# Performance work log

Measured on AMD Instinct MI355X. Metric: run time of the kernel, lower is better.

## Reference

```python
import jax, jax.numpy as jnp
import numpy as np

B, T, K = 256, 1024, 128


def setup_inputs() -> dict:
    key = jax.random.key(0)
    k1, k2, k3, k4, k5 = jax.random.split(key, 5)
    EMISSIONS = jax.random.normal(k1, (B, T, K), dtype=jnp.float32)
    TAGS = jax.random.randint(k2, (B, T), 0, K, dtype=jnp.int64)
    MASK = jnp.ones((B, T), dtype=bool)
    START = jax.random.normal(k3, (K,), dtype=jnp.float32) * 0.01
    END = jax.random.normal(k4, (K,), dtype=jnp.float32) * 0.01
    TRANS = jax.random.normal(k5, (K, K), dtype=jnp.float32) * 0.01
    return {"EMISSIONS": EMISSIONS, "TAGS": TAGS, "MASK": MASK,
            "START": START, "END": END, "TRANS": TRANS}


def _forward_logz(emissions, mask, start, end, trans):
    # emissions (B,T,K), mask (B,T) bool -> logZ (B,)
    alpha0 = start[None, :] + emissions[:, 0, :]  # (B,K)

    def step(alpha, inp):
        emit, m = inp  # emit (B,K), m (B,) bool
        # PACK[b,i,j] = alpha[b,i] + trans[i,j]; logsumexp over prev tag i
        new = jax.nn.logsumexp(alpha[:, :, None] + trans[None, :, :], axis=1) + emit
        alpha = jnp.where(m[:, None], new, alpha)
        return alpha, None

    xs = (jnp.swapaxes(emissions[:, 1:, :], 0, 1),  # (T-1,B,K)
          jnp.swapaxes(mask[:, 1:], 0, 1))          # (T-1,B)
    alphaT, _ = jax.lax.scan(step, alpha0, xs)
    return jax.nn.logsumexp(alphaT + end[None, :], axis=1)


def _gold_score(emissions, tags, mask, start, end, trans):
    b = emissions.shape[0]
    ba = jnp.arange(b)
    maskf = mask.astype(emissions.dtype)
    sc0 = (start[tags[:, 0]] + emissions[ba, 0, tags[:, 0]]) * maskf[:, 0]
    pr = jnp.maximum(tags[:, :-1], 0)  # clamp(min=0)
    cr = jnp.maximum(tags[:, 1:], 0)
    m = (mask[:, 1:] & mask[:, :-1]).astype(emissions.dtype)  # (B,T-1)
    trans_sc = trans[pr, cr]  # (B,T-1)
    emit_sc = jnp.take_along_axis(emissions[:, 1:, :], cr[:, :, None], axis=2)[:, :, 0]
    sc = sc0 + jnp.sum((trans_sc + emit_sc) * m, axis=1)
    lenm1 = jnp.sum(mask.astype(jnp.int32), axis=1) - 1
    last = tags[ba, lenm1]
    return sc + end[last]


def reference(EMISSIONS, TAGS, MASK, START, END, TRANS):
    logz = _forward_logz(EMISSIONS, MASK, START, END, TRANS)
    gold = _gold_score(EMISSIONS, TAGS, MASK, START, END, TRANS)
    return jnp.mean(logz - gold)
```

## Files before the change

kernel.cpp:

```cpp
#include <hip/hip_runtime.h>
#include <math.h>

#define Bn 256
#define Tn 1024
#define Kn 128
#define NT 256
#define CH 16
#define CHF (CH * Kn)
#define USTR 36
#define UW (4 * USTR)
#define UIDX(j) (((j) >> 5) * USTR + ((j) & 31))

__global__ __launch_bounds__(NT, 1) void crf_fwd_kernel(
    const float* __restrict__ emis,
    const int*   __restrict__ tags,
    const float* __restrict__ startv,
    const float* __restrict__ endv,
    const float* __restrict__ trans,
    float* __restrict__ per_b)
{
    const int b    = blockIdx.x;
    const int tid  = threadIdx.x;
    const int wave = tid >> 6;
    const int lane = tid & 63;
    const int g4   = lane >> 2;
    const int q    = lane & 3;
    const int c0   = wave * 32 + g4 * 2;
    const bool wrt = (q == 0);
    const int wslot = wave * USTR + 2 * g4;
    const int ubase = q * USTR;

    __shared__ __align__(16) float U[2 * UW];
    __shared__ __align__(16) float Xs[2 * CHF];
    __shared__ float red[NT];

    const float* eb = emis + (size_t)b * Tn * Kn;
    const int*   tb = tags + b * Tn;

    const float* tp = trans + (size_t)(32 * q) * Kn + c0;
    float4 F0, F1, F2, F3, F4, F5, F6, F7, F8, F9, F10, F11, F12, F13, F14, F15;
#define LDE(k, Fk)                                                  \
    {                                                               \
        float2 ea = *(const float2*)(tp + (size_t)(2 * k) * Kn);    \
        float2 ec = *(const float2*)(tp + (size_t)(2 * k + 1) * Kn);\
        Fk = make_float4(__expf(ea.x), __expf(ea.y),                \
                         __expf(ec.x), __expf(ec.y));               \
    }
    LDE(0, F0)   LDE(1, F1)   LDE(2, F2)   LDE(3, F3)
    LDE(4, F4)   LDE(5, F5)   LDE(6, F6)   LDE(7, F7)
    LDE(8, F8)   LDE(9, F9)   LDE(10, F10) LDE(11, F11)
    LDE(12, F12) LDE(13, F13) LDE(14, F14) LDE(15, F15)
#undef LDE

    float gl = 0.f;
    for (int t = 1 + tid; t < Tn; t += NT) {
        int pt = tb[t - 1];
        int ct = tb[t];
        gl += trans[pt * Kn + ct] + eb[(size_t)t * Kn + ct];
    }
    if (tid == 0) {
        int t0 = tb[0];
        gl += startv[t0] + eb[t0] + endv[tb[Tn - 1]];
    }
    red[tid] = gl;

    {
        const float4* e4 = (const float4*)(eb + Kn);
        float4 a = e4[tid];
        float4 d = e4[tid + NT];
        ((float4*)Xs)[tid] =
            make_float4(__expf(a.x), __expf(a.y), __expf(a.z), __expf(a.w));
        ((float4*)Xs)[tid + NT] =
            make_float4(__expf(d.x), __expf(d.y), __expf(d.z), __expf(d.w));
    }
    if (tid < Kn) {
        U[UW + UIDX(tid)] = __expf(startv[tid] + eb[tid]);
    }
    __syncthreads();

#pragma unroll
    for (int s = NT / 2; s > 0; s >>= 1) {
        if (tid < s) red[tid] += red[tid + s];
        __syncthreads();
    }
    const float gold = red[0];

    float  base = 0.f;
    float4 pf0  = make_float4(0, 0, 0, 0);
    float4 pf1  = make_float4(0, 0, 0, 0);

#define DOT2A(qa, qb, Fk)                      \
    aa0 = fmaf(qa, Fk.x, aa0);                 \
    aa1 = fmaf(qa, Fk.y, aa1);                 \
    ab0 = fmaf(qb, Fk.z, ab0);                 \
    ab1 = fmaf(qb, Fk.w, ab1);
#define DOT2B(qa, qb, Fk)                      \
    ba0 = fmaf(qa, Fk.x, ba0);                 \
    ba1 = fmaf(qa, Fk.y, ba1);                 \
    bb0 = fmaf(qb, Fk.z, bb0);                 \
    bb1 = fmaf(qb, Fk.w, bb1);

#define STEP(RB, SLOT, NORM)                                               \
    {                                                                      \
        const float4* Up4 = (const float4*)&U[(RB) * UW + ubase];          \
        float4 v0 = Up4[0], v1 = Up4[1], v2 = Up4[2], v3 = Up4[3];         \
        float4 v4 = Up4[4], v5 = Up4[5], v6 = Up4[6], v7 = Up4[7];         \
        float2 xr = *(const float2*)&Xc[(SLOT) * Kn + c0];                 \
        float u0 = 0.f, rn = 0.f;                                          \
        if (NORM) { u0 = U[(RB) * UW]; rn = __builtin_amdgcn_rcpf(u0); }   \
        float aa0 = 0.f, aa1 = 0.f, ab0 = 0.f, ab1 = 0.f;                  \
        float ba0 = 0.f, ba1 = 0.f, bb0 = 0.f, bb1 = 0.f;                  \
        DOT2A(v0.x, v0.y, F0)  DOT2A(v0.z, v0.w, F1)                       \
        DOT2A(v1.x, v1.y, F2)  DOT2A(v1.z, v1.w, F3)                       \
        DOT2A(v2.x, v2.y, F4)  DOT2A(v2.z, v2.w, F5)                       \
        DOT2A(v3.x, v3.y, F6)  DOT2A(v3.z, v3.w, F7)                       \
        DOT2B(v4.x, v4.y, F8)  DOT2B(v4.z, v4.w, F9)                       \
        DOT2B(v5.x, v5.y, F10) DOT2B(v5.z, v5.w, F11)                      \
        DOT2B(v6.x, v6.y, F12) DOT2B(v6.z, v6.w, F13)                      \
        DOT2B(v7.x, v7.y, F14) DOT2B(v7.z, v7.w, F15)                      \
        float m0 = ((aa0 + ab0) + (ba0 + bb0)) * xr.x;                     \
        float m1 = ((aa1 + ab1) + (ba1 + bb1)) * xr.y;                     \
        if (NORM) { m0 *= rn; m1 *= rn; base += __logf(u0); }              \
        int t_;                                                            \
        t_ = __builtin_amdgcn_mov_dpp(__float_as_int(m0), 0xB1, 0xF, 0xF, true); \
        m0 += __int_as_float(t_);                                          \
        t_ = __builtin_amdgcn_mov_dpp(__float_as_int(m1), 0xB1, 0xF, 0xF, true); \
        m1 += __int_as_float(t_);                                          \
        t_ = __builtin_amdgcn_mov_dpp(__float_as_int(m0), 0x4E, 0xF, 0xF, true); \
        m0 += __int_as_float(t_);                                          \
        t_ = __builtin_amdgcn_mov_dpp(__float_as_int(m1), 0x4E, 0xF, 0xF, true); \
        m1 += __int_as_float(t_);                                          \
        if (wrt) *(float2*)&U[((RB) ^ 1) * UW + wslot] = make_float2(m0, m1); \
        asm volatile("s_waitcnt lgkmcnt(0)" ::: "memory");                 \
        __builtin_amdgcn_s_barrier();                                      \
    }

    for (int cc = 0; cc < 63; ++cc) {
        const float* Xc = Xs + (cc & 1) * CHF;
        float*       Xn = (float*)Xs + ((cc & 1) ^ 1) * CHF;

        {
            const size_t base_el = (size_t)(16 * cc + 17) * Kn;
            const float4* s4 = (const float4*)(eb + base_el);
            pf0 = (base_el + (size_t)tid * 4 + 3 < (size_t)Tn * Kn)
                      ? s4[tid] : make_float4(0, 0, 0, 0);
            pf1 = (base_el + (size_t)(tid + NT) * 4 + 3 < (size_t)Tn * Kn)
                      ? s4[tid + NT] : make_float4(0, 0, 0, 0);
        }

        STEP(1, 0,  true ) STEP(0, 1,  false) STEP(1, 2,  false) STEP(0, 3,  false)
        STEP(1, 4,  true ) STEP(0, 5,  false) STEP(1, 6,  false) STEP(0, 7,  false)

        ((float4*)Xn)[tid] =
            make_float4(__expf(pf0.x), __expf(pf0.y), __expf(pf0.z), __expf(pf0.w));
        ((float4*)Xn)[tid + NT] =
            make_float4(__expf(pf1.x), __expf(pf1.y), __expf(pf1.z), __expf(pf1.w));

        STEP(1, 8,  true ) STEP(0, 9,  false) STEP(1, 10, false) STEP(0, 11, false)
        STEP(1, 12, true ) STEP(0, 13, false) STEP(1, 14, false) STEP(0, 15, false)
    }
    {
        const float* Xc = Xs + CHF;
        STEP(1, 0,  true ) STEP(0, 1,  false) STEP(1, 2,  false) STEP(0, 3,  false)
        STEP(1, 4,  true ) STEP(0, 5,  false) STEP(1, 6,  false) STEP(0, 7,  false)
        STEP(1, 8,  true ) STEP(0, 9,  false) STEP(1, 10, false) STEP(0, 11, false)
        STEP(1, 12, true ) STEP(0, 13, false) STEP(1, 14, false)
    }
#undef STEP
#undef DOT2A
#undef DOT2B

    float v = 0.f;
    if (tid < Kn) {
        float uT = U[UIDX(tid)];
        v = uT * __expf(endv[tid]);
    }
    red[tid] = v;
    __syncthreads();
#pragma unroll
    for (int s = NT / 2; s > 0; s >>= 1) {
        if (tid < s) red[tid] += red[tid + s];
        __syncthreads();
    }
    if (tid == 0)
        per_b[b] = base + __logf(red[0]) - gold;
}

__global__ __launch_bounds__(256) void crf_reduce(const float* __restrict__ per_b,
                                                  float* __restrict__ out) {
    __shared__ float red[256];
    int tid = threadIdx.x;
    red[tid] = per_b[tid];
    __syncthreads();
#pragma unroll
    for (int s = 128; s > 0; s >>= 1) {
        if (tid < s) red[tid] += red[tid + s];
        __syncthreads();
    }
    if (tid == 0) out[0] = red[0] * (1.0f / Bn);
}

extern "C" void kernel_launch(void* const* d_in, const int* in_sizes, int n_in,
                              void* d_out, int out_size, void* d_ws, size_t ws_size,
                              hipStream_t stream) {
    const float* emis   = (const float*)d_in[0];
    const int*   tags   = (const int*)d_in[1];
    const float* startv = (const float*)d_in[3];
    const float* endv   = (const float*)d_in[4];
    const float* trans  = (const float*)d_in[5];

    float* per_b = (float*)d_ws;

    crf_fwd_kernel<<<dim3(Bn), dim3(NT), 0, stream>>>(emis, tags, startv, endv,
                                                      trans, per_b);
    crf_reduce<<<dim3(1), dim3(256), 0, stream>>>(per_b, (float*)d_out);
}
```

Measured before the change: 463.6 us.

## Process two batch sequences per block with packed FMA and shared barriers

Each block now runs the forward recursion for two batch rows at once, interleaving their steps so that one barrier covers both sequences. The transition matrix is repacked into 2-wide vectors so the inner dot product can use packed FMA. The aim is to hide the per-step barrier and LDS latency of the serial recurrence with independent work, and to halve the VALU instruction count. In exchange the grid shrinks to 128 blocks on a device with more CUs than that, so half the CUs may sit idle, and register and LDS use per block roughly doubles.

```diff
diff --git a/kernel.cpp b/kernel.cpp
--- a/kernel.cpp
+++ b/kernel.cpp
@@ -11,6 +11,15 @@
 #define UW (4 * USTR)
 #define UIDX(j) (((j) >> 5) * USTR + ((j) & 31))
 
+typedef float v2f __attribute__((ext_vector_type(2)));
+
+__device__ __forceinline__ v2f mkv2(float a, float b) {
+    v2f r; r.x = a; r.y = b; return r;
+}
+__device__ __forceinline__ v2f pkfma(v2f a, v2f b, v2f c) {
+    return __builtin_elementwise_fma(a, b, c);
+}
+
 __global__ __launch_bounds__(NT, 1) void crf_fwd_kernel(
     const float* __restrict__ emis,
     const int*   __restrict__ tags,
@@ -19,7 +28,7 @@
     const float* __restrict__ trans,
     float* __restrict__ per_b)
 {
-    const int b    = blockIdx.x;
+    const int bb   = blockIdx.x;
     const int tid  = threadIdx.x;
     const int wave = tid >> 6;
     const int lane = tid & 63;
@@ -30,51 +39,60 @@
     const int wslot = wave * USTR + 2 * g4;
     const int ubase = q * USTR;
 
-    __shared__ __align__(16) float U[2 * UW];
-    __shared__ __align__(16) float Xs[2 * CHF];
+    __shared__ __align__(16) float U0[2 * UW];
+    __shared__ __align__(16) float U1[2 * UW];
+    __shared__ __align__(16) float X0[2 * CHF];
+    __shared__ __align__(16) float X1[2 * CHF];
     __shared__ float red[NT];
 
-    const float* eb = emis + (size_t)b * Tn * Kn;
-    const int*   tb = tags + b * Tn;
+    const float* eb0 = emis + (size_t)(2 * bb) * Tn * Kn;
+    const float* eb1 = eb0 + (size_t)Tn * Kn;
+    const int*   tb0 = tags + (2 * bb) * Tn;
+    const int*   tb1 = tb0 + Tn;
 
     const float* tp = trans + (size_t)(32 * q) * Kn + c0;
-    float4 F0, F1, F2, F3, F4, F5, F6, F7, F8, F9, F10, F11, F12, F13, F14, F15;
-#define LDE(k, Fk)                                                  \
-    {                                                               \
-        float2 ea = *(const float2*)(tp + (size_t)(2 * k) * Kn);    \
-        float2 ec = *(const float2*)(tp + (size_t)(2 * k + 1) * Kn);\
-        Fk = make_float4(__expf(ea.x), __expf(ea.y),                \
-                         __expf(ec.x), __expf(ec.y));               \
-    }
-    LDE(0, F0)   LDE(1, F1)   LDE(2, F2)   LDE(3, F3)
-    LDE(4, F4)   LDE(5, F5)   LDE(6, F6)   LDE(7, F7)
-    LDE(8, F8)   LDE(9, F9)   LDE(10, F10) LDE(11, F11)
-    LDE(12, F12) LDE(13, F13) LDE(14, F14) LDE(15, F15)
+    v2f GA0, GA1, GA2, GA3, GA4, GA5, GA6, GA7;
+    v2f GA8, GA9, GA10, GA11, GA12, GA13, GA14, GA15;
+    v2f GB0, GB1, GB2, GB3, GB4, GB5, GB6, GB7;
+    v2f GB8, GB9, GB10, GB11, GB12, GB13, GB14, GB15;
+#define LDE(n, GAn, GBn)                                        \
+    {                                                           \
+        float2 ra = *(const float2*)(tp + (size_t)(2*n) * Kn);  \
+        float2 rb = *(const float2*)(tp + (size_t)(2*n+1) * Kn);\
+        GAn = mkv2(__expf(ra.x), __expf(rb.x));                 \
+        GBn = mkv2(__expf(ra.y), __expf(rb.y));                 \
+    }
+    LDE(0, GA0, GB0)   LDE(1, GA1, GB1)   LDE(2, GA2, GB2)   LDE(3, GA3, GB3)
+    LDE(4, GA4, GB4)   LDE(5, GA5, GB5)   LDE(6, GA6, GB6)   LDE(7, GA7, GB7)
+    LDE(8, GA8, GB8)   LDE(9, GA9, GB9)   LDE(10, GA10, GB10) LDE(11, GA11, GB11)
+    LDE(12, GA12, GB12) LDE(13, GA13, GB13) LDE(14, GA14, GB14) LDE(15, GA15, GB15)
 #undef LDE
 
     float gl = 0.f;
     for (int t = 1 + tid; t < Tn; t += NT) {
-        int pt = tb[t - 1];
-        int ct = tb[t];
-        gl += trans[pt * Kn + ct] + eb[(size_t)t * Kn + ct];
+        gl += trans[tb0[t - 1] * Kn + tb0[t]] + eb0[(size_t)t * Kn + tb0[t]];
+        gl += trans[tb1[t - 1] * Kn + tb1[t]] + eb1[(size_t)t * Kn + tb1[t]];
     }
     if (tid == 0) {
-        int t0 = tb[0];
-        gl += startv[t0] + eb[t0] + endv[tb[Tn - 1]];
+        gl += startv[tb0[0]] + eb0[tb0[0]] + endv[tb0[Tn - 1]];
+        gl += startv[tb1[0]] + eb1[tb1[0]] + endv[tb1[Tn - 1]];
     }
     red[tid] = gl;
 
+#define EXP4(a) make_float4(__expf((a).x), __expf((a).y), __expf((a).z), __expf((a).w))
     {
-        const float4* e4 = (const float4*)(eb + Kn);
-        float4 a = e4[tid];
-        float4 d = e4[tid + NT];
-        ((float4*)Xs)[tid] =
-            make_float4(__expf(a.x), __expf(a.y), __expf(a.z), __expf(a.w));
-        ((float4*)Xs)[tid + NT] =
-            make_float4(__expf(d.x), __expf(d.y), __expf(d.z), __expf(d.w));
+        const float4* e4 = (const float4*)(eb0 + Kn);
+        float4 a = e4[tid], d = e4[tid + NT];
+        ((float4*)X0)[tid]      = EXP4(a);
+        ((float4*)X0)[tid + NT] = EXP4(d);
+        const float4* f4 = (const float4*)(eb1 + Kn);
+        a = f4[tid]; d = f4[tid + NT];
+        ((float4*)X1)[tid]      = EXP4(a);
+        ((float4*)X1)[tid + NT] = EXP4(d);
     }
     if (tid < Kn) {
-        U[UW + UIDX(tid)] = __expf(startv[tid] + eb[tid]);
+        U0[UW + UIDX(tid)] = __expf(startv[tid] + eb0[tid]);
+        U1[UW + UIDX(tid)] = __expf(startv[tid] + eb1[tid]);
     }
     __syncthreads();
 
@@ -83,44 +101,41 @@
         if (tid < s) red[tid] += red[tid + s];
         __syncthreads();
     }
-    const float gold = red[0];
-
-    float  base = 0.f;
-    float4 pf0  = make_float4(0, 0, 0, 0);
-    float4 pf1  = make_float4(0, 0, 0, 0);
-
-#define DOT2A(qa, qb, Fk)                      \
-    aa0 = fmaf(qa, Fk.x, aa0);                 \
-    aa1 = fmaf(qa, Fk.y, aa1);                 \
-    ab0 = fmaf(qb, Fk.z, ab0);                 \
-    ab1 = fmaf(qb, Fk.w, ab1);
-#define DOT2B(qa, qb, Fk)                      \
-    ba0 = fmaf(qa, Fk.x, ba0);                 \
-    ba1 = fmaf(qa, Fk.y, ba1);                 \
-    bb0 = fmaf(qb, Fk.z, bb0);                 \
-    bb1 = fmaf(qb, Fk.w, bb1);
-
-#define STEP(RB, SLOT, NORM)                                               \
+    const float gsum = red[0];
+
+    float base0 = 0.f, base1 = 0.f;
+    float4 pf00 = make_float4(0,0,0,0), pf01 = make_float4(0,0,0,0);
+    float4 pf10 = make_float4(0,0,0,0), pf11 = make_float4(0,0,0,0);
+
+#define DOTQ(qm, GAa, GAb, GBa, GBb)                    \
+    aA0 = pkfma(mkv2(qm.x, qm.y), GAa, aA0);            \
+    aB0 = pkfma(mkv2(qm.x, qm.y), GBa, aB0);            \
+    aA1 = pkfma(mkv2(qm.z, qm.w), GAb, aA1);            \
+    aB1 = pkfma(mkv2(qm.z, qm.w), GBb, aB1);
+
+#define STEP1(Ub, Xc, BASEV, RB, SLOT, NORM)                               \
     {                                                                      \
-        const float4* Up4 = (const float4*)&U[(RB) * UW + ubase];          \
-        float4 v0 = Up4[0], v1 = Up4[1], v2 = Up4[2], v3 = Up4[3];         \
-        float4 v4 = Up4[4], v5 = Up4[5], v6 = Up4[6], v7 = Up4[7];         \
+        const float4* Up4 = (const float4*)&Ub[(RB) * UW + ubase];         \
+        float4 q0 = Up4[0], q1 = Up4[1], q2 = Up4[2], q3 = Up4[3];         \
+        float4 q4 = Up4[4], q5 = Up4[5], q6 = Up4[6], q7 = Up4[7];         \
         float2 xr = *(const float2*)&Xc[(SLOT) * Kn + c0];                 \
         float u0 = 0.f, rn = 0.f;                                          \
-        if (NORM) { u0 = U[(RB) * UW]; rn = __builtin_amdgcn_rcpf(u0); }   \
-        float aa0 = 0.f, aa1 = 0.f, ab0 = 0.f, ab1 = 0.f;                  \
-        float ba0 = 0.f, ba1 = 0.f, bb0 = 0.f, bb1 = 0.f;                  \
-        DOT2A(v0.x, v0.y, F0)  DOT2A(v0.z, v0.w, F1)                       \
-        DOT2A(v1.x, v1.y, F2)  DOT2A(v1.z, v1.w, F3)                       \
-        DOT2A(v2.x, v2.y, F4)  DOT2A(v2.z, v2.w, F5)                       \
-        DOT2A(v3.x, v3.y, F6)  DOT2A(v3.z, v3.w, F7)                       \
-        DOT2B(v4.x, v4.y, F8)  DOT2B(v4.z, v4.w, F9)                       \
-        DOT2B(v5.x, v5.y, F10) DOT2B(v5.z, v5.w, F11)                      \
-        DOT2B(v6.x, v6.y, F12) DOT2B(v6.z, v6.w, F13)                      \
-        DOT2B(v7.x, v7.y, F14) DOT2B(v7.z, v7.w, F15)                      \
-        float m0 = ((aa0 + ab0) + (ba0 + bb0)) * xr.x;                     \
-        float m1 = ((aa1 + ab1) + (ba1 + bb1)) * xr.y;                     \
-        if (NORM) { m0 *= rn; m1 *= rn; base += __logf(u0); }              \
+        if (NORM) { u0 = Ub[(RB) * UW]; rn = __builtin_amdgcn_rcpf(u0); }  \
+        v2f aA0 = mkv2(0.f,0.f), aA1 = mkv2(0.f,0.f);                      \
+        v2f aB0 = mkv2(0.f,0.f), aB1 = mkv2(0.f,0.f);                      \
+        DOTQ(q0, GA0,  GA1,  GB0,  GB1)                                    \
+        DOTQ(q1, GA2,  GA3,  GB2,  GB3)                                    \
+        DOTQ(q2, GA4,  GA5,  GB4,  GB5)                                    \
+        DOTQ(q3, GA6,  GA7,  GB6,  GB7)                                    \
+        DOTQ(q4, GA8,  GA9,  GB8,  GB9)                                    \
+        DOTQ(q5, GA10, GA11, GB10, GB11)                                   \
+        DOTQ(q6, GA12, GA13, GB12, GB13)                                   \
+        DOTQ(q7, GA14, GA15, GB14, GB15)                                   \
+        v2f sA = aA0 + aA1;                                                \
+        v2f sB = aB0 + aB1;                                                \
+        float m0 = (sA.x + sA.y) * xr.x;                                   \
+        float m1 = (sB.x + sB.y) * xr.y;                                   \
+        if (NORM) { m0 *= rn; m1 *= rn; BASEV += __logf(u0); }             \
         int t_;                                                            \
         t_ = __builtin_amdgcn_mov_dpp(__float_as_int(m0), 0xB1, 0xF, 0xF, true); \
         m0 += __int_as_float(t_);                                          \
@@ -130,60 +145,78 @@
         m0 += __int_as_float(t_);                                          \
         t_ = __builtin_amdgcn_mov_dpp(__float_as_int(m1), 0x4E, 0xF, 0xF, true); \
         m1 += __int_as_float(t_);                                          \
-        if (wrt) *(float2*)&U[((RB) ^ 1) * UW + wslot] = make_float2(m0, m1); \
-        asm volatile("s_waitcnt lgkmcnt(0)" ::: "memory");                 \
-        __builtin_amdgcn_s_barrier();                                      \
-    }
+        if (wrt) *(float2*)&Ub[((RB) ^ 1) * UW + wslot] = make_float2(m0, m1); \
+    }
+
+#define PAIR(RB, SLOT, NORM)                                               \
+    STEP1(U0, Xc0, base0, RB, SLOT, NORM)                                  \
+    STEP1(U1, Xc1, base1, RB, SLOT, NORM)                                  \
+    asm volatile("s_waitcnt lgkmcnt(0)" ::: "memory");                     \
+    __builtin_amdgcn_s_barrier();
 
     for (int cc = 0; cc < 63; ++cc) {
-        const float* Xc = Xs + (cc & 1) * CHF;
-        float*       Xn = (float*)Xs + ((cc & 1) ^ 1) * CHF;
+        const float* Xc0 = X0 + (cc & 1) * CHF;
+        const float* Xc1 = X1 + (cc & 1) * CHF;
+        float* Xn0 = (float*)X0 + ((cc & 1) ^ 1) * CHF;
+        float* Xn1 = (float*)X1 + ((cc & 1) ^ 1) * CHF;
 
         {
             const size_t base_el = (size_t)(16 * cc + 17) * Kn;
-            const float4* s4 = (const float4*)(eb + base_el);
-            pf0 = (base_el + (size_t)tid * 4 + 3 < (size_t)Tn * Kn)
-                      ? s4[tid] : make_float4(0, 0, 0, 0);
-            pf1 = (base_el + (size_t)(tid + NT) * 4 + 3 < (size_t)Tn * Kn)
-                      ? s4[tid + NT] : make_float4(0, 0, 0, 0);
+            const float4* s40 = (const float4*)(eb0 + base_el);
+            const float4* s41 = (const float4*)(eb1 + base_el);
+            bool ok0 = base_el + (size_t)tid * 4 + 3 < (size_t)Tn * Kn;
+            bool ok1 = base_el + (size_t)(tid + NT) * 4 + 3 < (size_t)Tn * Kn;
+            pf00 = ok0 ? s40[tid]      : make_float4(0,0,0,0);
+            pf01 = ok1 ? s40[tid + NT] : make_float4(0,0,0,0);
+            pf10 = ok0 ? s41[tid]      : make_float4(0,0,0,0);
+            pf11 = ok1 ? s41[tid + NT] : make_float4(0,0,0,0);
         }
 
-        STEP(1, 0,  true ) STEP(0, 1,  false) STEP(1, 2,  false) STEP(0, 3,  false)
-        STEP(1, 4,  true ) STEP(0, 5,  false) STEP(1, 6,  false) STEP(0, 7,  false)
-
-        ((float4*)Xn)[tid] =
-            make_float4(__expf(pf0.x), __expf(pf0.y), __expf(pf0.z), __expf(pf0.w));
-        ((float4*)Xn)[tid + NT] =
-            make_float4(__expf(pf1.x), __expf(pf1.y), __expf(pf1.z), __expf(pf1.w));
-
-        STEP(1, 8,  true ) STEP(0, 9,  false) STEP(1, 10, false) STEP(0, 11, false)
-        STEP(1, 12, true ) STEP(0, 13, false) STEP(1, 14, false) STEP(0, 15, false)
+        PAIR(1, 0,  true ) PAIR(0, 1,  false) PAIR(1, 2,  false) PAIR(0, 3,  false)
+        PAIR(1, 4,  true ) PAIR(0, 5,  false) PAIR(1, 6,  false) PAIR(0, 7,  false)
+
+        ((float4*)Xn0)[tid]      = EXP4(pf00);
+        ((float4*)Xn0)[tid + NT] = EXP4(pf01);
+        ((float4*)Xn1)[tid]      = EXP4(pf10);
+        ((float4*)Xn1)[tid + NT] = EXP4(pf11);
+
+        PAIR(1, 8,  true ) PAIR(0, 9,  false) PAIR(1, 10, false) PAIR(0, 11, false)
+        PAIR(1, 12, true ) PAIR(0, 13, false) PAIR(1, 14, false) PAIR(0, 15, false)
     }
     {
-        const float* Xc = Xs + CHF;
-        STEP(1, 0,  true ) STEP(0, 1,  false) STEP(1, 2,  false) STEP(0, 3,  false)
-        STEP(1, 4,  true ) STEP(0, 5,  false) STEP(1, 6,  false) STEP(0, 7,  false)
-        STEP(1, 8,  true ) STEP(0, 9,  false) STEP(1, 10, false) STEP(0, 11, false)
-        STEP(1, 12, true ) STEP(0, 13, false) STEP(1, 14, false)
-    }
-#undef STEP
-#undef DOT2A
-#undef DOT2B
-
-    float v = 0.f;
-    if (tid < Kn) {
-        float uT = U[UIDX(tid)];
-        v = uT * __expf(endv[tid]);
-    }
-    red[tid] = v;
+        const float* Xc0 = X0 + CHF;
+        const float* Xc1 = X1 + CHF;
+        PAIR(1, 0,  true ) PAIR(0, 1,  false) PAIR(1, 2,  false) PAIR(0, 3,  false)
+        PAIR(1, 4,  true ) PAIR(0, 5,  false) PAIR(1, 6,  false) PAIR(0, 7,  false)
+        PAIR(1, 8,  true ) PAIR(0, 9,  false) PAIR(1, 10, false) PAIR(0, 11, false)
+        PAIR(1, 12, true ) PAIR(0, 13, false) PAIR(1, 14, false)
+    }
+#undef PAIR
+#undef STEP1
+#undef DOTQ
+#undef EXP4
+
+    float ev = (tid < Kn) ? __expf(endv[tid]) : 0.f;
+    red[tid] = (tid < Kn) ? U0[UIDX(tid)] * ev : 0.f;
     __syncthreads();
 #pragma unroll
     for (int s = NT / 2; s > 0; s >>= 1) {
         if (tid < s) red[tid] += red[tid + s];
         __syncthreads();
     }
-    if (tid == 0)
-        per_b[b] = base + __logf(red[0]) - gold;
+    const float z0 = red[0];
+    __syncthreads();
+    red[tid] = (tid < Kn) ? U1[UIDX(tid)] * ev : 0.f;
+    __syncthreads();
+#pragma unroll
+    for (int s = NT / 2; s > 0; s >>= 1) {
+        if (tid < s) red[tid] += red[tid + s];
+        __syncthreads();
+    }
+    if (tid == 0) {
+        per_b[2 * bb]     = base0 + __logf(z0) + base1 + __logf(red[0]) - gsum;
+        per_b[2 * bb + 1] = 0.f;
+    }
 }
 
 __global__ __launch_bounds__(256) void crf_reduce(const float* __restrict__ per_b,
@@ -211,7 +244,7 @@
 
     float* per_b = (float*)d_ws;
 
-    crf_fwd_kernel<<<dim3(Bn), dim3(NT), 0, stream>>>(emis, tags, startv, endv,
-                                                      trans, per_b);
+    crf_fwd_kernel<<<dim3(Bn / 2), dim3(NT), 0, stream>>>(emis, tags, startv,
+                                                          endv, trans, per_b);
     crf_reduce<<<dim3(1), dim3(256), 0, stream>>>(per_b, (float*)d_out);
 }
```

Measured after the change: 706.1 us. +52.3%, slower.
